# Optimization experiments

Hardware: AMD Instinct MI355X
Metric: run time of the kernel (lower is better)

## Reference

```python
import jax, jax.numpy as jnp
import numpy as np

E = 8      # n_routed_experts
TOPK = 2
D = 768    # hidden_dim
F = 3072   # routed_expert_inter_dim (== shared_expert_inter_dim)


def setup_inputs() -> dict:
    key = jax.random.key(0)
    ks = jax.random.split(key, 11)
    s = 0.02
    return {
        "x": jax.random.normal(ks[0], (2, 64, 64, D), dtype=jnp.float32),
        "gate_w": jax.random.normal(ks[1], (E, D), dtype=jnp.float32),          # Gate.weight (torch randn init)
        "w1": jax.random.normal(ks[2], (E, F, D), dtype=jnp.float32) * s,       # Expert.fc1.weight per expert
        "b1": jax.random.normal(ks[3], (E, F), dtype=jnp.float32) * s,
        "w2": jax.random.normal(ks[4], (E, D, F), dtype=jnp.float32) * s,       # Expert.fc2.weight per expert
        "b2": jax.random.normal(ks[5], (E, D), dtype=jnp.float32) * s,
        "ws1": jax.random.normal(ks[6], (F, D), dtype=jnp.float32) * s,         # shared GeluMLP fc1
        "bs1": jax.random.normal(ks[7], (F,), dtype=jnp.float32) * s,
        "ws2": jax.random.normal(ks[8], (D, F), dtype=jnp.float32) * s,         # shared GeluMLP fc2
        "bs2": jax.random.normal(ks[9], (D,), dtype=jnp.float32) * s,
    }


def _gelu(v):
    return jax.nn.gelu(v, approximate=False)  # torch nn.GELU default = exact erf


def reference(x, gate_w, w1, b1, w2, b2, ws1, bs1, ws2, bs2):
    B, H, W, Dh = x.shape
    xf = x.reshape(-1, Dh)                                  # [T, D]
    T = xf.shape[0]

    # Gate: softmax over expert logits, top-k, renormalize
    scores = jax.nn.softmax(xf @ gate_w.T, axis=-1)         # [T, E]
    vals, idx = jax.lax.top_k(scores, TOPK)                 # [T, K]
    vals = vals / jnp.sum(vals, axis=-1, keepdims=True)

    # Dense combine weights: 0 for unselected experts (faithful to scatter-add)
    cw = jnp.zeros((T, E), dtype=xf.dtype).at[
        jnp.arange(T)[:, None], idx
    ].add(vals)                                             # [T, E]

    # Routed experts: small fixed structural loop over E experts
    out = jnp.zeros_like(xf)
    for e in range(E):
        h = _gelu(xf @ w1[e].T + b1[e])                     # [T, F]
        y = h @ w2[e].T + b2[e]                             # [T, D]
        out = out + y * cw[:, e:e + 1]

    # Shared expert (GeluMLP) applied to all tokens
    shared = _gelu(xf @ ws1.T + bs1) @ ws2.T + bs2          # [T, D]

    return (out + shared).reshape(B, H, W, Dh)
```

## Files before the change

kernel.cpp:

```cpp
#include <hip/hip_runtime.h>
#include <hip/hip_bf16.h>

#define T_TOK 8192
#define E_EXP 8
#define DDIM  768
#define FDIM  3072

typedef _Float16 f16x8 __attribute__((ext_vector_type(8)));
typedef _Float16 f16x4 __attribute__((ext_vector_type(4)));
typedef float    f32x4 __attribute__((ext_vector_type(4)));

static const size_t XH_OFF   = 0;
static const size_t W1H_OFF  = 12582912;
static const size_t Y_OFF    = W1H_OFF;
static const size_t W2H_OFF  = 50331648;
static const size_t WS1H_OFF = 88080384;
static const size_t WS2H_OFF = 92798976;
static const size_t H_OFF    = 97517568;
static const size_t ROWS_OFF = 198180864;
static const size_t RW_OFF   = 198246400;
static const size_t TIDX_OFF = 198311936;
static const size_t TW_OFF   = 198377472;
static const size_t CNT_OFF  = 198443008;
static const size_t BASE_OFF = 198443264;
static const size_t CUR_OFF  = 198443520;
static const size_t TSLOT_OFF= 198443776;
static const size_t WS_NEED  = 198509312;

__device__ inline float fast_gelu(float v) {
    float v2 = v * v;
    float z2n = v * __builtin_fmaf(v2, -0.0713548163f, -1.5957691216f);
    float e = __expf(z2n);
    float s = __builtin_amdgcn_rcpf(1.0f + e);
    return v * s;
}

__global__ void cvt_f32_f16(const float* __restrict__ src, _Float16* __restrict__ dst, int n4) {
    int i = blockIdx.x * blockDim.x + threadIdx.x;
    if (i >= n4) return;
    float4 v = ((const float4*)src)[i];
    f16x4 o = { (_Float16)v.x, (_Float16)v.y, (_Float16)v.z, (_Float16)v.w };
    *(f16x4*)(dst + 4 * (size_t)i) = o;
}

__global__ void gate_kernel(const float* __restrict__ x, const float* __restrict__ gw,
                            int* __restrict__ tidx, float* __restrict__ tw) {
    int wave = threadIdx.x >> 6;
    int lane = threadIdx.x & 63;
    int t = blockIdx.x * 4 + wave;
    const float4* xv = (const float4*)(x + (size_t)t * DDIM);
    float p[E_EXP];
#pragma unroll
    for (int e = 0; e < E_EXP; e++) p[e] = 0.f;
    for (int i = lane; i < DDIM / 4; i += 64) {
        float4 xv4 = xv[i];
#pragma unroll
        for (int e = 0; e < E_EXP; e++) {
            float4 g = ((const float4*)(gw + (size_t)e * DDIM))[i];
            p[e] += xv4.x * g.x + xv4.y * g.y + xv4.z * g.z + xv4.w * g.w;
        }
    }
#pragma unroll
    for (int e = 0; e < E_EXP; e++) {
#pragma unroll
        for (int off = 32; off; off >>= 1) p[e] += __shfl_xor(p[e], off);
    }
    if (lane == 0) {
        int i0 = 0;
#pragma unroll
        for (int e = 1; e < E_EXP; e++) if (p[e] > p[i0]) i0 = e;
        int i1 = (i0 == 0) ? 1 : 0;
#pragma unroll
        for (int e = 0; e < E_EXP; e++) {
            if (e == i0) continue;
            if (p[e] > p[i1]) i1 = e;
        }
        float d  = p[i1] - p[i0];
        float e1 = expf(d);
        float w0 = 1.f / (1.f + e1);
        float w1 = 1.f - w0;
        tidx[2 * t]     = i0;  tw[2 * t]     = w0;
        tidx[2 * t + 1] = i1;  tw[2 * t + 1] = w1;
    }
}

__global__ void count_kernel(const int* __restrict__ tidx, int* __restrict__ cnt,
                             int* __restrict__ base, int* __restrict__ cur) {
    int c[E_EXP];
#pragma unroll
    for (int e = 0; e < E_EXP; e++) c[e] = 0;
    for (int i = threadIdx.x; i < 2 * T_TOK; i += 1024) {
        int e = tidx[i];
#pragma unroll
        for (int k = 0; k < E_EXP; k++) c[k] += (e == k) ? 1 : 0;
    }
#pragma unroll
    for (int e = 0; e < E_EXP; e++) {
#pragma unroll
        for (int off = 32; off; off >>= 1) c[e] += __shfl_xor(c[e], off);
    }
    __shared__ int wsum[16][E_EXP];
    int lane = threadIdx.x & 63, wave = threadIdx.x >> 6;
    if (lane == 0) {
#pragma unroll
        for (int e = 0; e < E_EXP; e++) wsum[wave][e] = c[e];
    }
    __syncthreads();
    if (threadIdx.x == 0) {
        int acc = 0;
        for (int e = 0; e < E_EXP; e++) {
            int s = 0;
            for (int w = 0; w < 16; w++) s += wsum[w][e];
            cnt[e] = s; base[e] = acc; cur[e] = acc; acc += s;
        }
    }
}

__global__ void scatter_kernel(const int* __restrict__ tidx, const float* __restrict__ tw,
                               int* __restrict__ cur, int* __restrict__ rowsIdx,
                               float* __restrict__ rw, int* __restrict__ tslot) {
    int t = blockIdx.x * 256 + threadIdx.x;
    int lane = threadIdx.x & 63, wave = threadIdx.x >> 6;
    unsigned long long lt = ((unsigned long long)1 << lane) - 1ull;
    __shared__ int wcnt[8][E_EXP];
    __shared__ int wpre[8][E_EXP];
    __shared__ int bbase[E_EXP];

    int myE[2], myR[2];
#pragma unroll
    for (int k = 0; k < 2; k++) {
        int e = tidx[2 * t + k];
        myE[k] = e;
        int vw = wave * 2 + k;
        int rank = 0;
#pragma unroll
        for (int ee = 0; ee < E_EXP; ee++) {
            unsigned long long m = __ballot(e == ee);
            if (e == ee) rank = __builtin_popcountll(m & lt);
            if (lane == 0) wcnt[vw][ee] = __builtin_popcountll(m);
        }
        myR[k] = rank;
    }
    __syncthreads();
    if (threadIdx.x < E_EXP) {
        int e = threadIdx.x, acc = 0;
#pragma unroll
        for (int vw = 0; vw < 8; vw++) { wpre[vw][e] = acc; acc += wcnt[vw][e]; }
        bbase[e] = atomicAdd(&cur[e], acc);
    }
    __syncthreads();
#pragma unroll
    for (int k = 0; k < 2; k++) {
        int e = myE[k];
        int slot = bbase[e] + wpre[wave * 2 + k][e] + myR[k];
        rowsIdx[slot] = t;
        rw[slot] = tw[2 * t + k];
        tslot[2 * t + k] = slot;
    }
}

__global__ void combine_kernel(const _Float16* __restrict__ y,
                               const int* __restrict__ tslot,
                               float* __restrict__ out) {
    int idx = blockIdx.x * 256 + threadIdx.x;
    int t = idx / (DDIM / 8);
    int c = (idx % (DDIM / 8)) * 8;
    int s0 = tslot[2 * t], s1 = tslot[2 * t + 1];
    f16x8 a = *(const f16x8*)(y + (size_t)s0 * DDIM + c);
    f16x8 b = *(const f16x8*)(y + (size_t)s1 * DDIM + c);
    float4* o = (float4*)(out + (size_t)t * DDIM + c);
    float4 o0 = o[0], o1 = o[1];
    o0.x += (float)a[0] + (float)b[0];
    o0.y += (float)a[1] + (float)b[1];
    o0.z += (float)a[2] + (float)b[2];
    o0.w += (float)a[3] + (float)b[3];
    o1.x += (float)a[4] + (float)b[4];
    o1.y += (float)a[5] + (float)b[5];
    o1.z += (float)a[6] + (float)b[6];
    o1.w += (float)a[7] + (float)b[7];
    o[0] = o0; o[1] = o1;
}

#define FC1S 0
#define FC2S 1
#define FC1R 2
#define FC2R 3

template <int MODE>
__global__ __launch_bounds__(256, 2) void gemm_kernel(
    const _Float16* __restrict__ Abase,
    const _Float16* __restrict__ Wbase,
    const float* __restrict__ biasBase,
    _Float16* __restrict__ h,
    float* __restrict__ out,
    const int* __restrict__ cnt, const int* __restrict__ base,
    const int* __restrict__ rowsIdx, const float* __restrict__ rw)
{
    constexpr int K = (MODE == FC1S || MODE == FC1R) ? DDIM : FDIM;
    constexpr int N = (MODE == FC1S || MODE == FC1R) ? FDIM : DDIM;
    constexpr bool ROUTED = (MODE == FC1R || MODE == FC2R);

    int m0, mEnd;
    const _Float16* W;
    const float* bias;
    if constexpr (ROUTED) {
        int bx = blockIdx.x, accb = 0, expert = -1, rb = 0;
#pragma unroll
        for (int e = 0; e < E_EXP; e++) {
            int nb = (cnt[e] + 127) >> 7;
            if (expert < 0 && bx < accb + nb) { expert = e; rb = bx - accb; }
            accb += nb;
        }
        if (expert < 0) return;
        m0   = base[expert] + rb * 128;
        mEnd = base[expert] + cnt[expert];
        W    = Wbase + (size_t)expert * N * K;
        bias = biasBase + (size_t)expert * N;
    } else {
        m0 = blockIdx.x * 128;
        mEnd = T_TOK;
        W = Wbase;
        bias = biasBase;
    }
    int n0 = blockIdx.y * 128;

    __shared__ __align__(16) _Float16 As[128 * 64];
    __shared__ __align__(16) _Float16 Bs[128 * 64];

    int tid  = threadIdx.x;
    int lane = tid & 63;
    int wid  = tid >> 6;
    int wm   = wid >> 1, wn = wid & 1;
    int m16  = lane & 15, q = lane >> 4;
    int x7   = m16 & 7;

    f32x4 acc[4][4];
#pragma unroll
    for (int i = 0; i < 4; i++)
#pragma unroll
        for (int j = 0; j < 4; j++) acc[i][j] = f32x4{0.f, 0.f, 0.f, 0.f};

    const _Float16* ap[4];
    const _Float16* bp[4];
#pragma unroll
    for (int tse = 0; tse < 4; tse++) {
        int L = wid * 256 + tse * 64 + lane;
        int r = L >> 3;
        int c = (L & 7) ^ (r & 7);
        int pr = m0 + r;
        bool valid = pr < mEnd;
        int ar;
        if constexpr (MODE == FC1R) ar = rowsIdx[valid ? pr : m0];
        else                        ar = valid ? pr : m0;
        ap[tse] = Abase + (size_t)ar * K + c * 8;
        bp[tse] = W + (size_t)(n0 + r) * K + c * 8;
    }

    for (int k0 = 0; k0 < K; k0 += 64) {
#pragma unroll
        for (int tse = 0; tse < 4; tse++) {
            __builtin_amdgcn_global_load_lds(
                (const __attribute__((address_space(1))) void*)ap[tse],
                (__attribute__((address_space(3))) void*)(As + wid * 2048 + tse * 512),
                16, 0, 0);
            ap[tse] += 64;
        }
#pragma unroll
        for (int tse = 0; tse < 4; tse++) {
            __builtin_amdgcn_global_load_lds(
                (const __attribute__((address_space(1))) void*)bp[tse],
                (__attribute__((address_space(3))) void*)(Bs + wid * 2048 + tse * 512),
                16, 0, 0);
            bp[tse] += 64;
        }
        __syncthreads();
#pragma unroll
        for (int ks = 0; ks < 2; ks++) {
            f16x8 af[4], bf[4];
#pragma unroll
            for (int i = 0; i < 4; i++)
                af[i] = *(const f16x8*)(As + (wm * 64 + i * 16 + m16) * 64 + (((ks * 4 + q) ^ x7) * 8));
#pragma unroll
            for (int j = 0; j < 4; j++)
                bf[j] = *(const f16x8*)(Bs + (wn * 64 + j * 16 + m16) * 64 + (((ks * 4 + q) ^ x7) * 8));
#pragma unroll
            for (int i = 0; i < 4; i++)
#pragma unroll
                for (int j = 0; j < 4; j++)
                    acc[i][j] = __builtin_amdgcn_mfma_f32_16x16x32_f16(af[i], bf[j], acc[i][j], 0, 0, 0);
        }
        __syncthreads();
    }

    float biasv[4];
#pragma unroll
    for (int j = 0; j < 4; j++) biasv[j] = bias[n0 + wn * 64 + j * 16 + m16];

#pragma unroll
    for (int i = 0; i < 4; i++) {
#pragma unroll
        for (int r = 0; r < 4; r++) {
            int rowp = m0 + wm * 64 + i * 16 + q * 4 + r;
            if (rowp >= mEnd) continue;
            float wgt = 0.f;
            if constexpr (MODE == FC2R) wgt = rw[rowp];
#pragma unroll
            for (int j = 0; j < 4; j++) {
                int col = n0 + wn * 64 + j * 16 + m16;
                float v = acc[i][j][r] + biasv[j];
                if constexpr (MODE == FC1S || MODE == FC1R) {
                    v = fast_gelu(v);
                    h[(size_t)rowp * FDIM + col] = (_Float16)v;
                } else if constexpr (MODE == FC2S) {
                    out[(size_t)rowp * DDIM + col] = v;
                } else {
                    h[(size_t)rowp * DDIM + col] = (_Float16)(v * wgt);
                }
            }
        }
    }
}

extern "C" void kernel_launch(void* const* d_in, const int* in_sizes, int n_in,
                              void* d_out, int out_size, void* d_ws, size_t ws_size,
                              hipStream_t stream) {
    const float* x   = (const float*)d_in[0];
    const float* gw  = (const float*)d_in[1];
    const float* w1  = (const float*)d_in[2];
    const float* b1  = (const float*)d_in[3];
    const float* w2  = (const float*)d_in[4];
    const float* b2  = (const float*)d_in[5];
    const float* ws1 = (const float*)d_in[6];
    const float* bs1 = (const float*)d_in[7];
    const float* ws2 = (const float*)d_in[8];
    const float* bs2 = (const float*)d_in[9];
    float* out = (float*)d_out;
    char* ws = (char*)d_ws;
    if (ws_size < WS_NEED) return;

    _Float16* xh   = (_Float16*)(ws + XH_OFF);
    _Float16* w1h  = (_Float16*)(ws + W1H_OFF);
    _Float16* yb   = (_Float16*)(ws + Y_OFF);
    _Float16* w2h  = (_Float16*)(ws + W2H_OFF);
    _Float16* ws1h = (_Float16*)(ws + WS1H_OFF);
    _Float16* ws2h = (_Float16*)(ws + WS2H_OFF);
    _Float16* h    = (_Float16*)(ws + H_OFF);
    int*   rowsIdx = (int*)(ws + ROWS_OFF);
    float* rw      = (float*)(ws + RW_OFF);
    int*   tidx    = (int*)(ws + TIDX_OFF);
    float* tw      = (float*)(ws + TW_OFF);
    int*   cnt     = (int*)(ws + CNT_OFF);
    int*   base    = (int*)(ws + BASE_OFF);
    int*   cur     = (int*)(ws + CUR_OFF);
    int*   tslot   = (int*)(ws + TSLOT_OFF);

    cvt_f32_f16<<<6144,  256, 0, stream>>>(x,   xh,   1572864);
    cvt_f32_f16<<<18432, 256, 0, stream>>>(w1,  w1h,  4718592);
    cvt_f32_f16<<<18432, 256, 0, stream>>>(w2,  w2h,  4718592);
    cvt_f32_f16<<<2304,  256, 0, stream>>>(ws1, ws1h, 589824);
    cvt_f32_f16<<<2304,  256, 0, stream>>>(ws2, ws2h, 589824);

    gate_kernel<<<2048, 256, 0, stream>>>(x, gw, tidx, tw);
    count_kernel<<<1, 1024, 0, stream>>>(tidx, cnt, base, cur);
    scatter_kernel<<<32, 256, 0, stream>>>(tidx, tw, cur, rowsIdx, rw, tslot);

    gemm_kernel<FC1S><<<dim3(64, 24),  256, 0, stream>>>(xh, ws1h, bs1, h, out, cnt, base, rowsIdx, rw);
    gemm_kernel<FC2S><<<dim3(64, 6),   256, 0, stream>>>(h,  ws2h, bs2, h, out, cnt, base, rowsIdx, rw);
    gemm_kernel<FC1R><<<dim3(136, 24), 256, 0, stream>>>(xh, w1h,  b1,  h, out, cnt, base, rowsIdx, rw);
    gemm_kernel<FC2R><<<dim3(136, 6),  256, 0, stream>>>(h,  w2h,  b2,  yb, out, cnt, base, rowsIdx, rw);

    combine_kernel<<<3072, 256, 0, stream>>>(yb, tslot, out);
}
```

Measured before the change: 582.7 us.

## Rewrite GEMM as 256x128 tile, 8-wave, multi-buffered LDS pipeline with setprio

Restructures the GEMM kernel to use 512-thread blocks computing 256x128 tiles, with a 128KB shared buffer split into double-buffered A stages and quad-buffered B stages. Global-to-LDS loads are issued ahead of the MFMA work and partially awaited with vmcnt waits, and s_setprio raises wave priority around the MFMA bursts. The goal is to hide memory latency and raise reuse per block. The cost is more LDS per block, which lowers occupancy, and more padded rows in the routed expert tiles.

```diff
diff --git a/kernel.cpp b/kernel.cpp
--- a/kernel.cpp
+++ b/kernel.cpp
@@ -186,8 +186,48 @@
 #define FC1R 2
 #define FC2R 3
 
+#define GLL(srcp, ldsoff) __builtin_amdgcn_global_load_lds( \
+    (const __attribute__((address_space(1))) void*)(srcp), \
+    (__attribute__((address_space(3))) void*)(sm + (ldsoff)), 16, 0, 0)
+
+#define STAGE_A(b, koff) do { \
+    GLL(pA[0] + (koff), (b)*16384 +         wid*512); \
+    GLL(pA[1] + (koff), (b)*16384 +  4096 + wid*512); \
+    GLL(pA[2] + (koff), (b)*16384 +  8192 + wid*512); \
+    GLL(pA[3] + (koff), (b)*16384 + 12288 + wid*512); \
+} while (0)
+
+#define STAGE_B(sl, koff) do { \
+    GLL(pB[0] + (koff), 32768 + (sl)*8192 +        wid*512); \
+    GLL(pB[1] + (koff), 32768 + (sl)*8192 + 4096 + wid*512); \
+} while (0)
+
+#define LDA(b) do { _Pragma("unroll") for (int i = 0; i < 4; i++) { \
+    af[i][0] = *(const f16x8*)(sm + (b)*16384 + aRd + i*1024 + ch0); \
+    af[i][1] = *(const f16x8*)(sm + (b)*16384 + aRd + i*1024 + ch1); } \
+} while (0)
+
+#define LDB(sl, jlo) do { \
+    bf[(jlo)  ][0] = *(const f16x8*)(sm + bRd + (sl)*8192 + ((jlo)  )*1024 + ch0); \
+    bf[(jlo)  ][1] = *(const f16x8*)(sm + bRd + (sl)*8192 + ((jlo)  )*1024 + ch1); \
+    bf[(jlo)+1][0] = *(const f16x8*)(sm + bRd + (sl)*8192 + ((jlo)+1)*1024 + ch0); \
+    bf[(jlo)+1][1] = *(const f16x8*)(sm + bRd + (sl)*8192 + ((jlo)+1)*1024 + ch1); \
+} while (0)
+
+#define MM(jlo) do { _Pragma("unroll") for (int i = 0; i < 4; i++) { \
+    acc[i][(jlo)  ] = __builtin_amdgcn_mfma_f32_16x16x32_f16(af[i][0], bf[(jlo)  ][0], acc[i][(jlo)  ], 0,0,0); \
+    acc[i][(jlo)+1] = __builtin_amdgcn_mfma_f32_16x16x32_f16(af[i][0], bf[(jlo)+1][0], acc[i][(jlo)+1], 0,0,0); \
+    acc[i][(jlo)  ] = __builtin_amdgcn_mfma_f32_16x16x32_f16(af[i][1], bf[(jlo)  ][1], acc[i][(jlo)  ], 0,0,0); \
+    acc[i][(jlo)+1] = __builtin_amdgcn_mfma_f32_16x16x32_f16(af[i][1], bf[(jlo)+1][1], acc[i][(jlo)+1], 0,0,0); } \
+} while (0)
+
+#define BARRIER __builtin_amdgcn_s_barrier()
+#define PRIO1 __builtin_amdgcn_s_setprio(1)
+#define PRIO0 __builtin_amdgcn_s_setprio(0)
+#define VM6 asm volatile("s_waitcnt vmcnt(6)" ::: "memory")
+
 template <int MODE>
-__global__ __launch_bounds__(256, 2) void gemm_kernel(
+__global__ __launch_bounds__(512, 2) void gemm_kernel(
     const _Float16* __restrict__ Abase,
     const _Float16* __restrict__ Wbase,
     const float* __restrict__ biasBase,
@@ -199,6 +239,7 @@
     constexpr int K = (MODE == FC1S || MODE == FC1R) ? DDIM : FDIM;
     constexpr int N = (MODE == FC1S || MODE == FC1R) ? FDIM : DDIM;
     constexpr bool ROUTED = (MODE == FC1R || MODE == FC2R);
+    constexpr int NI2 = K / 256;
 
     int m0, mEnd;
     const _Float16* W;
@@ -207,30 +248,30 @@
         int bx = blockIdx.x, accb = 0, expert = -1, rb = 0;
 #pragma unroll
         for (int e = 0; e < E_EXP; e++) {
-            int nb = (cnt[e] + 127) >> 7;
+            int nb = (cnt[e] + 255) >> 8;
             if (expert < 0 && bx < accb + nb) { expert = e; rb = bx - accb; }
             accb += nb;
         }
         if (expert < 0) return;
-        m0   = base[expert] + rb * 128;
+        m0   = base[expert] + rb * 256;
         mEnd = base[expert] + cnt[expert];
         W    = Wbase + (size_t)expert * N * K;
         bias = biasBase + (size_t)expert * N;
     } else {
-        m0 = blockIdx.x * 128;
+        m0 = blockIdx.x * 256;
         mEnd = T_TOK;
         W = Wbase;
         bias = biasBase;
     }
     int n0 = blockIdx.y * 128;
 
-    __shared__ __align__(16) _Float16 As[128 * 64];
-    __shared__ __align__(16) _Float16 Bs[128 * 64];
+    __shared__ __align__(16) _Float16 sm[65536];
 
     int tid  = threadIdx.x;
     int lane = tid & 63;
     int wid  = tid >> 6;
-    int wm   = wid >> 1, wn = wid & 1;
+    int wm   = wid >> 1;
+    int wn   = wid & 1;
     int m16  = lane & 15, q = lane >> 4;
     int x7   = m16 & 7;
 
@@ -240,57 +281,75 @@
 #pragma unroll
         for (int j = 0; j < 4; j++) acc[i][j] = f32x4{0.f, 0.f, 0.f, 0.f};
 
-    const _Float16* ap[4];
-    const _Float16* bp[4];
-#pragma unroll
-    for (int tse = 0; tse < 4; tse++) {
-        int L = wid * 256 + tse * 64 + lane;
-        int r = L >> 3;
-        int c = (L & 7) ^ (r & 7);
-        int pr = m0 + r;
+    int r0  = tid >> 3;
+    int cSw = (tid & 7) ^ (r0 & 7);
+    const _Float16* pA[4];
+    const _Float16* pB[2];
+#pragma unroll
+    for (int j = 0; j < 4; j++) {
+        int tr = (j >> 1) * 128 + (j & 1) * 64 + r0;
+        int pr = m0 + tr;
         bool valid = pr < mEnd;
         int ar;
         if constexpr (MODE == FC1R) ar = rowsIdx[valid ? pr : m0];
         else                        ar = valid ? pr : m0;
-        ap[tse] = Abase + (size_t)ar * K + c * 8;
-        bp[tse] = W + (size_t)(n0 + r) * K + c * 8;
-    }
-
-    for (int k0 = 0; k0 < K; k0 += 64) {
-#pragma unroll
-        for (int tse = 0; tse < 4; tse++) {
-            __builtin_amdgcn_global_load_lds(
-                (const __attribute__((address_space(1))) void*)ap[tse],
-                (__attribute__((address_space(3))) void*)(As + wid * 2048 + tse * 512),
-                16, 0, 0);
-            ap[tse] += 64;
-        }
-#pragma unroll
-        for (int tse = 0; tse < 4; tse++) {
-            __builtin_amdgcn_global_load_lds(
-                (const __attribute__((address_space(1))) void*)bp[tse],
-                (__attribute__((address_space(3))) void*)(Bs + wid * 2048 + tse * 512),
-                16, 0, 0);
-            bp[tse] += 64;
-        }
-        __syncthreads();
-#pragma unroll
-        for (int ks = 0; ks < 2; ks++) {
-            f16x8 af[4], bf[4];
-#pragma unroll
-            for (int i = 0; i < 4; i++)
-                af[i] = *(const f16x8*)(As + (wm * 64 + i * 16 + m16) * 64 + (((ks * 4 + q) ^ x7) * 8));
-#pragma unroll
-            for (int j = 0; j < 4; j++)
-                bf[j] = *(const f16x8*)(Bs + (wn * 64 + j * 16 + m16) * 64 + (((ks * 4 + q) ^ x7) * 8));
-#pragma unroll
-            for (int i = 0; i < 4; i++)
-#pragma unroll
-                for (int j = 0; j < 4; j++)
-                    acc[i][j] = __builtin_amdgcn_mfma_f32_16x16x32_f16(af[i], bf[j], acc[i][j], 0, 0, 0);
-        }
-        __syncthreads();
-    }
+        pA[j] = Abase + (size_t)ar * K + cSw * 8;
+    }
+#pragma unroll
+    for (int s = 0; s < 2; s++)
+        pB[s] = W + (size_t)(n0 + s * 64 + r0) * K + cSw * 8;
+
+    int aRd = (wm >> 1) * 8192 + ((wm & 1) * 64 + m16) * 64;
+    int bRd = 32768 + (wn * 64 + m16) * 64;
+    int ch0 = (q ^ x7) * 8;
+    int ch1 = ((4 + q) ^ x7) * 8;
+
+    f16x8 af[4][2], bf[4][2];
+
+    STAGE_A(0, 0);
+    STAGE_B(0, 0);
+    STAGE_A(1, 64);
+    STAGE_B(1, 64);
+#pragma unroll
+    for (int j = 0; j < 4; j++) pA[j] += 128;
+#pragma unroll
+    for (int s = 0; s < 2; s++) pB[s] += 128;
+    asm volatile("s_waitcnt vmcnt(6)" ::: "memory");
+    BARRIER;
+
+#pragma unroll 1
+    for (int tt = 0; tt < NI2; ++tt) {
+        LDA(0); LDB(0, 0); STAGE_B(2, 0);
+        BARRIER; PRIO1; MM(0); PRIO0; BARRIER;
+
+        LDB(0, 2); STAGE_A(0, 0);
+        BARRIER; PRIO1; MM(2); PRIO0; VM6; BARRIER;
+
+        LDA(1); LDB(1, 0); STAGE_B(3, 64);
+        BARRIER; PRIO1; MM(0); PRIO0; BARRIER;
+
+        LDB(1, 2); STAGE_A(1, 64);
+        BARRIER; PRIO1; MM(2); PRIO0; VM6; BARRIER;
+
+        LDA(0); LDB(2, 0); STAGE_B(0, 128);
+        BARRIER; PRIO1; MM(0); PRIO0; BARRIER;
+
+        LDB(2, 2); STAGE_A(0, 128);
+        BARRIER; PRIO1; MM(2); PRIO0; VM6; BARRIER;
+
+        LDA(1); LDB(3, 0); STAGE_B(1, 192);
+        BARRIER; PRIO1; MM(0); PRIO0; BARRIER;
+
+        LDB(3, 2); STAGE_A(1, 192);
+        BARRIER; PRIO1; MM(2); PRIO0; VM6; BARRIER;
+
+#pragma unroll
+        for (int j = 0; j < 4; j++) pA[j] += 256;
+#pragma unroll
+        for (int s = 0; s < 2; s++) pB[s] += 256;
+    }
+
+    asm volatile("s_waitcnt vmcnt(0)" ::: "memory");
 
     float biasv[4];
 #pragma unroll
@@ -320,6 +379,17 @@
         }
     }
 }
+
+#undef GLL
+#undef STAGE_A
+#undef STAGE_B
+#undef LDA
+#undef LDB
+#undef MM
+#undef BARRIER
+#undef PRIO1
+#undef PRIO0
+#undef VM6
 
 extern "C" void kernel_launch(void* const* d_in, const int* in_sizes, int n_in,
                               void* d_out, int out_size, void* d_ws, size_t ws_size,
@@ -364,10 +434,10 @@
     count_kernel<<<1, 1024, 0, stream>>>(tidx, cnt, base, cur);
     scatter_kernel<<<32, 256, 0, stream>>>(tidx, tw, cur, rowsIdx, rw, tslot);
 
-    gemm_kernel<FC1S><<<dim3(64, 24),  256, 0, stream>>>(xh, ws1h, bs1, h, out, cnt, base, rowsIdx, rw);
-    gemm_kernel<FC2S><<<dim3(64, 6),   256, 0, stream>>>(h,  ws2h, bs2, h, out, cnt, base, rowsIdx, rw);
-    gemm_kernel<FC1R><<<dim3(136, 24), 256, 0, stream>>>(xh, w1h,  b1,  h, out, cnt, base, rowsIdx, rw);
-    gemm_kernel<FC2R><<<dim3(136, 6),  256, 0, stream>>>(h,  w2h,  b2,  yb, out, cnt, base, rowsIdx, rw);
+    gemm_kernel<FC1S><<<dim3(32, 24), 512, 0, stream>>>(xh, ws1h, bs1, h, out, cnt, base, rowsIdx, rw);
+    gemm_kernel<FC2S><<<dim3(32, 6),  512, 0, stream>>>(h,  ws2h, bs2, h, out, cnt, base, rowsIdx, rw);
+    gemm_kernel<FC1R><<<dim3(72, 24), 512, 0, stream>>>(xh, w1h,  b1,  h, out, cnt, base, rowsIdx, rw);
+    gemm_kernel<FC2R><<<dim3(72, 6),  512, 0, stream>>>(h,  w2h,  b2,  yb, out, cnt, base, rowsIdx, rw);
 
     combine_kernel<<<3072, 256, 0, stream>>>(yb, tslot, out);
 }
```

Measured after the change: 611.0 us. 4.9% more time.

## Rewrite GEMM as 256x256 tile with 4-stage LDS pipeline and 8 waves

Applied to the files above, without the earlier changes.

Grows the GEMM block tile from 128x128 to 256x256 with 512 threads (8 waves, each computing 128x64), shrinks the K step to 32, and adds a 4-slot LDS ring with direct-to-LDS loads issued two stages ahead. Loads are interleaved with MFMA halves using raw barriers, vmcnt waits and setprio. The aim is to hide global-load latency and raise operand reuse per LDS load. In exchange it uses 128 KB of LDS per block and a larger accumulator register set, which limits occupancy, and gives fewer blocks for the smaller GEMMs.

```diff
diff --git a/kernel.cpp b/kernel.cpp
--- a/kernel.cpp
+++ b/kernel.cpp
@@ -186,8 +186,22 @@
 #define FC1R 2
 #define FC2R 3
 
+#define GLL(p, off16) __builtin_amdgcn_global_load_lds( \
+    (const __attribute__((address_space(1))) void*)(p), \
+    (__attribute__((address_space(3))) void*)(sm + (off16)), 16, 0, 0)
+
+#define STAGE_A(sl, ko) do { \
+    GLL(pA0 + (ko), (sl)*8192 +        wid*512); \
+    GLL(pA1 + (ko), (sl)*8192 + 4096 + wid*512); \
+} while (0)
+
+#define STAGE_B(sl, ko) do { \
+    GLL(pB0 + (ko), 32768 + (sl)*8192 +        wid*512); \
+    GLL(pB1 + (ko), 32768 + (sl)*8192 + 4096 + wid*512); \
+} while (0)
+
 template <int MODE>
-__global__ __launch_bounds__(256, 2) void gemm_kernel(
+__global__ __launch_bounds__(512, 2) void gemm_kernel(
     const _Float16* __restrict__ Abase,
     const _Float16* __restrict__ Wbase,
     const float* __restrict__ biasBase,
@@ -199,6 +213,7 @@
     constexpr int K = (MODE == FC1S || MODE == FC1R) ? DDIM : FDIM;
     constexpr int N = (MODE == FC1S || MODE == FC1R) ? FDIM : DDIM;
     constexpr bool ROUTED = (MODE == FC1R || MODE == FC2R);
+    constexpr int NT = K / 32;
 
     int m0, mEnd;
     const _Float16* W;
@@ -207,100 +222,115 @@
         int bx = blockIdx.x, accb = 0, expert = -1, rb = 0;
 #pragma unroll
         for (int e = 0; e < E_EXP; e++) {
-            int nb = (cnt[e] + 127) >> 7;
+            int nb = (cnt[e] + 255) >> 8;
             if (expert < 0 && bx < accb + nb) { expert = e; rb = bx - accb; }
             accb += nb;
         }
         if (expert < 0) return;
-        m0   = base[expert] + rb * 128;
+        m0   = base[expert] + rb * 256;
         mEnd = base[expert] + cnt[expert];
         W    = Wbase + (size_t)expert * N * K;
         bias = biasBase + (size_t)expert * N;
     } else {
-        m0 = blockIdx.x * 128;
+        m0 = blockIdx.x * 256;
         mEnd = T_TOK;
         W = Wbase;
         bias = biasBase;
     }
-    int n0 = blockIdx.y * 128;
-
-    __shared__ __align__(16) _Float16 As[128 * 64];
-    __shared__ __align__(16) _Float16 Bs[128 * 64];
+    int n0 = blockIdx.y * 256;
+
+    __shared__ __align__(16) _Float16 sm[65536];
 
     int tid  = threadIdx.x;
     int lane = tid & 63;
     int wid  = tid >> 6;
-    int wm   = wid >> 1, wn = wid & 1;
+    int wm   = wid >> 2;
+    int wn   = wid & 3;
     int m16  = lane & 15, q = lane >> 4;
-    int x7   = m16 & 7;
-
-    f32x4 acc[4][4];
-#pragma unroll
-    for (int i = 0; i < 4; i++)
+    int x3   = m16 & 3;
+
+    f32x4 acc[8][4];
+#pragma unroll
+    for (int i = 0; i < 8; i++)
 #pragma unroll
         for (int j = 0; j < 4; j++) acc[i][j] = f32x4{0.f, 0.f, 0.f, 0.f};
 
-    const _Float16* ap[4];
-    const _Float16* bp[4];
-#pragma unroll
-    for (int tse = 0; tse < 4; tse++) {
-        int L = wid * 256 + tse * 64 + lane;
-        int r = L >> 3;
-        int c = (L & 7) ^ (r & 7);
-        int pr = m0 + r;
-        bool valid = pr < mEnd;
-        int ar;
-        if constexpr (MODE == FC1R) ar = rowsIdx[valid ? pr : m0];
-        else                        ar = valid ? pr : m0;
-        ap[tse] = Abase + (size_t)ar * K + c * 8;
-        bp[tse] = W + (size_t)(n0 + r) * K + c * 8;
-    }
-
-    for (int k0 = 0; k0 < K; k0 += 64) {
-#pragma unroll
-        for (int tse = 0; tse < 4; tse++) {
-            __builtin_amdgcn_global_load_lds(
-                (const __attribute__((address_space(1))) void*)ap[tse],
-                (__attribute__((address_space(3))) void*)(As + wid * 2048 + tse * 512),
-                16, 0, 0);
-            ap[tse] += 64;
-        }
-#pragma unroll
-        for (int tse = 0; tse < 4; tse++) {
-            __builtin_amdgcn_global_load_lds(
-                (const __attribute__((address_space(1))) void*)bp[tse],
-                (__attribute__((address_space(3))) void*)(Bs + wid * 2048 + tse * 512),
-                16, 0, 0);
-            bp[tse] += 64;
-        }
-        __syncthreads();
-#pragma unroll
-        for (int ks = 0; ks < 2; ks++) {
-            f16x8 af[4], bf[4];
-#pragma unroll
-            for (int i = 0; i < 4; i++)
-                af[i] = *(const f16x8*)(As + (wm * 64 + i * 16 + m16) * 64 + (((ks * 4 + q) ^ x7) * 8));
+    int r0  = tid >> 2;
+    int cSw = (tid & 3) ^ (r0 & 3);
+    const _Float16 *pA0, *pA1, *pB0, *pB1;
+    {
+        int pr0 = m0 + r0,       pr1 = m0 + 128 + r0;
+        bool v0 = pr0 < mEnd,    v1 = pr1 < mEnd;
+        int ar0, ar1;
+        if constexpr (MODE == FC1R) {
+            ar0 = rowsIdx[v0 ? pr0 : m0];
+            ar1 = rowsIdx[v1 ? pr1 : m0];
+        } else {
+            ar0 = v0 ? pr0 : m0;
+            ar1 = v1 ? pr1 : m0;
+        }
+        pA0 = Abase + (size_t)ar0 * K + cSw * 8;
+        pA1 = Abase + (size_t)ar1 * K + cSw * 8;
+    }
+    pB0 = W + (size_t)(n0 +       r0) * K + cSw * 8;
+    pB1 = W + (size_t)(n0 + 128 + r0) * K + cSw * 8;
+
+    int aRd = (wm * 128 + m16) * 32 + (q ^ x3) * 8;
+    int bRd = 32768 + (wn * 64 + m16) * 32 + (q ^ x3) * 8;
+
+    STAGE_A(0, 0);  STAGE_B(0, 0);
+    STAGE_A(1, 32); STAGE_B(1, 32);
+    asm volatile("s_waitcnt vmcnt(4)" ::: "memory");
+    __builtin_amdgcn_s_barrier();
+
+#pragma unroll 4
+    for (int t = 0; t < NT; ++t) {
+        int sl = t & 3, s2 = (t + 2) & 3;
+        f16x8 af[4], bf[4];
+#pragma unroll
+        for (int j = 0; j < 4; j++)
+            bf[j] = *(const f16x8*)(sm + sl * 8192 + bRd + j * 512);
+#pragma unroll
+        for (int i = 0; i < 4; i++)
+            af[i] = *(const f16x8*)(sm + sl * 8192 + aRd + i * 512);
+        STAGE_A(s2, 64);
+        __builtin_amdgcn_s_barrier();
+        __builtin_amdgcn_s_setprio(1);
+#pragma unroll
+        for (int i = 0; i < 4; i++)
 #pragma unroll
             for (int j = 0; j < 4; j++)
-                bf[j] = *(const f16x8*)(Bs + (wn * 64 + j * 16 + m16) * 64 + (((ks * 4 + q) ^ x7) * 8));
-#pragma unroll
-            for (int i = 0; i < 4; i++)
-#pragma unroll
-                for (int j = 0; j < 4; j++)
-                    acc[i][j] = __builtin_amdgcn_mfma_f32_16x16x32_f16(af[i], bf[j], acc[i][j], 0, 0, 0);
-        }
-        __syncthreads();
-    }
+                acc[i][j] = __builtin_amdgcn_mfma_f32_16x16x32_f16(af[i], bf[j], acc[i][j], 0, 0, 0);
+        __builtin_amdgcn_s_setprio(0);
+        __builtin_amdgcn_s_barrier();
+#pragma unroll
+        for (int i = 0; i < 4; i++)
+            af[i] = *(const f16x8*)(sm + sl * 8192 + aRd + (4 + i) * 512);
+        STAGE_B(s2, 64);
+        __builtin_amdgcn_s_barrier();
+        __builtin_amdgcn_s_setprio(1);
+#pragma unroll
+        for (int i = 0; i < 4; i++)
+#pragma unroll
+            for (int j = 0; j < 4; j++)
+                acc[4 + i][j] = __builtin_amdgcn_mfma_f32_16x16x32_f16(af[i], bf[j], acc[4 + i][j], 0, 0, 0);
+        __builtin_amdgcn_s_setprio(0);
+        asm volatile("s_waitcnt vmcnt(4)" ::: "memory");
+        __builtin_amdgcn_s_barrier();
+        pA0 += 32; pA1 += 32; pB0 += 32; pB1 += 32;
+    }
+
+    asm volatile("s_waitcnt vmcnt(0)" ::: "memory");
 
     float biasv[4];
 #pragma unroll
     for (int j = 0; j < 4; j++) biasv[j] = bias[n0 + wn * 64 + j * 16 + m16];
 
 #pragma unroll
-    for (int i = 0; i < 4; i++) {
+    for (int i = 0; i < 8; i++) {
 #pragma unroll
         for (int r = 0; r < 4; r++) {
-            int rowp = m0 + wm * 64 + i * 16 + q * 4 + r;
+            int rowp = m0 + wm * 128 + i * 16 + q * 4 + r;
             if (rowp >= mEnd) continue;
             float wgt = 0.f;
             if constexpr (MODE == FC2R) wgt = rw[rowp];
@@ -320,6 +350,10 @@
         }
     }
 }
+
+#undef GLL
+#undef STAGE_A
+#undef STAGE_B
 
 extern "C" void kernel_launch(void* const* d_in, const int* in_sizes, int n_in,
                               void* d_out, int out_size, void* d_ws, size_t ws_size,
@@ -364,10 +398,10 @@
     count_kernel<<<1, 1024, 0, stream>>>(tidx, cnt, base, cur);
     scatter_kernel<<<32, 256, 0, stream>>>(tidx, tw, cur, rowsIdx, rw, tslot);
 
-    gemm_kernel<FC1S><<<dim3(64, 24),  256, 0, stream>>>(xh, ws1h, bs1, h, out, cnt, base, rowsIdx, rw);
-    gemm_kernel<FC2S><<<dim3(64, 6),   256, 0, stream>>>(h,  ws2h, bs2, h, out, cnt, base, rowsIdx, rw);
-    gemm_kernel<FC1R><<<dim3(136, 24), 256, 0, stream>>>(xh, w1h,  b1,  h, out, cnt, base, rowsIdx, rw);
-    gemm_kernel<FC2R><<<dim3(136, 6),  256, 0, stream>>>(h,  w2h,  b2,  yb, out, cnt, base, rowsIdx, rw);
+    gemm_kernel<FC1S><<<dim3(32, 12), 512, 0, stream>>>(xh, ws1h, bs1, h, out, cnt, base, rowsIdx, rw);
+    gemm_kernel<FC2S><<<dim3(32, 3),  512, 0, stream>>>(h,  ws2h, bs2, h, out, cnt, base, rowsIdx, rw);
+    gemm_kernel<FC1R><<<dim3(72, 12), 512, 0, stream>>>(xh, w1h,  b1,  h, out, cnt, base, rowsIdx, rw);
+    gemm_kernel<FC2R><<<dim3(72, 3),  512, 0, stream>>>(h,  w2h,  b2,  yb, out, cnt, base, rowsIdx, rw);
 
     combine_kernel<<<3072, 256, 0, stream>>>(yb, tslot, out);
 }
```

New measurement: 631.4 us. +8.4%, slower.
